# Optimization experiments

Hardware: AMD Instinct MI355X
Metric: run time of the kernel (lower is better)

The kernel has to match this reference:

```python
import jax, jax.numpy as jnp
import numpy as np

N = 8192
IN_DIM = 256
OUT_DIM = 256
NEG_INF = -9e15


def setup_inputs() -> dict:
    key = jax.random.key(0)
    k1, k2, k3, k4, k5 = jax.random.split(key, 5)
    worker_x = jax.random.normal(k1, (N, IN_DIM), dtype=jnp.float32)
    ww_adj = jax.random.randint(k2, (N, N), 0, 2, dtype=jnp.int32)
    # learned params (xavier-ish scales)
    W = jax.random.normal(k3, (IN_DIM, OUT_DIM), dtype=jnp.float32) * (1.0 / np.sqrt(IN_DIM))
    a_src = jax.random.normal(k4, (OUT_DIM, 1), dtype=jnp.float32) * (1.414 / np.sqrt(OUT_DIM))
    a_dst = jax.random.normal(k5, (OUT_DIM, 1), dtype=jnp.float32) * (1.414 / np.sqrt(OUT_DIM))
    return {"worker_x": worker_x, "ww_adj": ww_adj, "W": W, "a_src": a_src, "a_dst": a_dst}


def reference(worker_x, ww_adj, W, a_src, a_dst):
    Wh = worker_x @ W                       # [N, out_dim]
    f_src = Wh @ a_src                      # [N, 1]
    f_dst = Wh @ a_dst                      # [N, 1]
    e = jax.nn.leaky_relu(f_src + f_dst.T, negative_slope=0.2)  # [N, N]
    attention = jnp.where(ww_adj > 0, e, NEG_INF)
    attention = jax.nn.softmax(attention, axis=-1)
    h_prime = attention @ Wh                # [N, out_dim]
    return jax.nn.elu(h_prime)
```

## Files before the change

### kernel.cpp

```cpp
#include <hip/hip_runtime.h>
#include <stdint.h>

typedef __attribute__((ext_vector_type(8))) short short8;
typedef __attribute__((ext_vector_type(4))) float f32x4;
typedef __attribute__((ext_vector_type(4))) _Float16 h16x4;

#define LOG2E 1.4426950408889634f

#define OFF_WTT   0u
#define OFF_WHTB  131072u
#define OFF_BITS  4325376u
#define OFF_FSRC  12713984u
#define OFF_FDST  12746752u
#define OFF_MKEY  12779520u
#define OFF_LP    12779584u
#define OFF_ACCH  13041728u

__device__ __forceinline__ unsigned short f2bf(float f) {
    union { float f; unsigned int i; } v; v.f = f;
    unsigned int u = v.i;
    return (unsigned short)((u + 0x7FFFu + ((u >> 16) & 1u)) >> 16);
}

__global__ void k0_init(const float* __restrict__ W,
                        unsigned short* __restrict__ WTt,
                        unsigned int* __restrict__ Mkey) {
    int idx = blockIdx.x * 256 + threadIdx.x;
    int i = idx >> 8, o = idx & 255;
    WTt[(i >> 5) * 8192 + ((i >> 3) & 3) * 2048 + o * 8 + (i & 7)] = f2bf(W[idx]);
    if (idx == 0) *Mkey = 0u;
}

__global__ __launch_bounds__(256, 8)
void k_pack(const int* __restrict__ adj, unsigned long long* __restrict__ bits64) {
    int wave_id = (blockIdx.x * 256 + threadIdx.x) >> 6;
    int lane = threadIdx.x & 63;
    const int* p = adj + (size_t)wave_id * 16384 + lane;
    unsigned long long* bp = bits64 + (size_t)wave_id * 256;
    for (int it = 0; it < 256; it += 8) {
        int v[8];
#pragma unroll
        for (int u = 0; u < 8; ++u) v[u] = p[(size_t)(it + u) * 64];
#pragma unroll
        for (int u = 0; u < 8; ++u) {
            unsigned long long m = __ballot(v[u] > 0);
            if (lane == 0) bp[it + u] = m;
        }
    }
}

__global__ __launch_bounds__(256, 2)
void k1_stage1(const float* __restrict__ X,
               const unsigned short* __restrict__ WTt,
               const float* __restrict__ a_src,
               const float* __restrict__ a_dst,
               unsigned short* __restrict__ WhTb,
               float* __restrict__ f_src,
               float* __restrict__ f_dst,
               unsigned int* __restrict__ Mkey) {
    __shared__ __align__(16) unsigned short Bt[8192];
    __shared__ float fsum[64];
    const int t = threadIdx.x, w = t >> 6, lane = t & 63, l15 = lane & 15, q = lane >> 4;
    const int rg = w & 1, cg = w >> 1;
    const int i0 = blockIdx.x * 32;
    const int arow = i0 + rg * 16 + l15;

    if (t < 64) fsum[t] = 0.f;

    float as[8], ad[8];
#pragma unroll
    for (int ci = 0; ci < 8; ++ci) {
        int col = cg * 128 + ci * 16 + l15;
        as[ci] = a_src[col]; ad[ci] = a_dst[col];
    }

    f32x4 acc[8];
#pragma unroll
    for (int ci = 0; ci < 8; ++ci) acc[ci] = (f32x4)0.f;

    for (int ks = 0; ks < 8; ++ks) {
        __syncthreads();
        {
            const uint4* src = (const uint4*)(WTt + ks * 8192);
            uint4* dst = (uint4*)Bt;
            dst[t] = src[t]; dst[256 + t] = src[256 + t];
            dst[512 + t] = src[512 + t]; dst[768 + t] = src[768 + t];
        }
        __syncthreads();
        const float* xp = X + (size_t)arow * 256 + ks * 32 + q * 8;
        float4 xa = *(const float4*)xp;
        float4 xb = *(const float4*)(xp + 4);
        short8 a;
        a[0] = (short)f2bf(xa.x); a[1] = (short)f2bf(xa.y);
        a[2] = (short)f2bf(xa.z); a[3] = (short)f2bf(xa.w);
        a[4] = (short)f2bf(xb.x); a[5] = (short)f2bf(xb.y);
        a[6] = (short)f2bf(xb.z); a[7] = (short)f2bf(xb.w);
#pragma unroll
        for (int ci = 0; ci < 8; ++ci) {
            short8 b = *(const short8*)((const char*)Bt + q * 4096 + (cg * 128 + ci * 16 + l15) * 16);
            acc[ci] = __builtin_amdgcn_mfma_f32_16x16x32_bf16(a, b, acc[ci], 0, 0, 0);
        }
    }

#pragma unroll
    for (int ci = 0; ci < 8; ++ci) {
        int col = cg * 128 + ci * 16 + l15;
        ushort4 v;
        v.x = f2bf(acc[ci][0]); v.y = f2bf(acc[ci][1]);
        v.z = f2bf(acc[ci][2]); v.w = f2bf(acc[ci][3]);
        size_t flat = (size_t)(i0 >> 5) * 8192 + (size_t)(rg * 2 + (q >> 1)) * 2048
                      + (size_t)col * 8 + (q & 1) * 4;
        *(ushort4*)(WhTb + flat) = v;
    }

#pragma unroll
    for (int reg = 0; reg < 4; ++reg) {
        float ps = 0.f, pd = 0.f;
#pragma unroll
        for (int ci = 0; ci < 8; ++ci) {
            ps += acc[ci][reg] * as[ci];
            pd += acc[ci][reg] * ad[ci];
        }
#pragma unroll
        for (int m = 1; m < 16; m <<= 1) {
            ps += __shfl_xor(ps, m, 64);
            pd += __shfl_xor(pd, m, 64);
        }
        if (l15 == 0) {
            atomicAdd(&fsum[rg * 16 + q * 4 + reg], ps);
            atomicAdd(&fsum[32 + rg * 16 + q * 4 + reg], pd);
        }
    }
    __syncthreads();
    if (t < 32) {
        int row = i0 + t;
        float ps = fsum[t], pd = fsum[32 + t];
        f_src[row] = ps;
        f_dst[row] = pd;
        union { float f; unsigned int u; } cv; cv.f = pd;
        unsigned int key = (cv.u & 0x80000000u) ? ~cv.u : (cv.u | 0x80000000u);
        atomicMax(Mkey, key);
    }
}

__global__ __launch_bounds__(256, 2)
void k2_flash(const unsigned int* __restrict__ BITS,
              const unsigned short* __restrict__ WhTb,
              const float* __restrict__ f_src,
              const float* __restrict__ f_dst,
              const unsigned int* __restrict__ Mkey,
              float* __restrict__ Lp,
              _Float16* __restrict__ ACCh) {
    __shared__ float fd_s[1024];
    __shared__ unsigned int bits_s[128 * 33];
    const int t = threadIdx.x, w = t >> 6, lane = t & 63, l15 = lane & 15, q = lane >> 4;
    const int i0 = blockIdx.x * 128;
    const int jc = blockIdx.y;
    const int jb0 = jc * 1024;
    const int jw0 = jc * 32;

    { float4* d = (float4*)fd_s; d[t] = ((const float4*)(f_dst + jb0))[t]; }
#pragma unroll
    for (int s = 0; s < 16; ++s) {
        int idx = s * 256 + t;
        int row = idx >> 5, word = idx & 31;
        bits_s[row * 33 + word] = BITS[(size_t)(i0 + row) * 256 + jw0 + word];
    }

    unsigned int key = *Mkey;
    union { unsigned int u; float f; } mv;
    mv.u = (key & 0x80000000u) ? (key & 0x7FFFFFFFu) : ~key;
    const float Mf = mv.f;
    const int rA = i0 + w * 32 + l15;
    const float fsA = f_src[rA], fsB = f_src[rA + 16];
    float vA = fsA + Mf; const float mcA = fmaxf(vA, 0.2f * vA) * LOG2E;
    float vB = fsB + Mf; const float mcB = fmaxf(vB, 0.2f * vB) * LOG2E;
    __syncthreads();

    const unsigned short* Bbase = WhTb + (size_t)jw0 * 8192 + q * 2048 + l15 * 8;
    const unsigned int* brA = &bits_s[(w * 32 + l15) * 33];
    const unsigned int* brB = &bits_s[(w * 32 + 16 + l15) * 33];

    f32x4 accA[16], accB[16];
#pragma unroll
    for (int ci = 0; ci < 16; ++ci) { accA[ci] = (f32x4)0.f; accB[ci] = (f32x4)0.f; }
    float lsA = 0.f, lsB = 0.f;

    for (int js = 0; js < 32; ++js) {
        const float* fdp = fd_s + js * 32 + q * 8;
        float4 f0 = *(const float4*)fdp, f1 = *(const float4*)(fdp + 4);
        float fdv[8] = { f0.x, f0.y, f0.z, f0.w, f1.x, f1.y, f1.z, f1.w };
        unsigned int bA = brA[js] >> (q * 8);
        unsigned int bB = brB[js] >> (q * 8);

        short8 fragA, fragB;
#pragma unroll
        for (int k = 0; k < 8; ++k) {
            float tA = fsA + fdv[k];
            float eA = fmaxf(tA, 0.2f * tA);
            float pA = __builtin_amdgcn_exp2f(__builtin_fmaf(eA, LOG2E, -mcA));
            pA = ((bA >> k) & 1u) ? pA : 0.f;
            lsA += pA; fragA[k] = (short)f2bf(pA);
            float tB = fsB + fdv[k];
            float eB = fmaxf(tB, 0.2f * tB);
            float pB = __builtin_amdgcn_exp2f(__builtin_fmaf(eB, LOG2E, -mcB));
            pB = ((bB >> k) & 1u) ? pB : 0.f;
            lsB += pB; fragB[k] = (short)f2bf(pB);
        }

        const unsigned short* bp = Bbase + (size_t)js * 8192;
        short8 bf[8];
#pragma unroll
        for (int ci = 0; ci < 8; ++ci) bf[ci] = *(const short8*)(bp + ci * 128);
#pragma unroll
        for (int ci = 0; ci < 8; ++ci) {
            accA[ci] = __builtin_amdgcn_mfma_f32_16x16x32_bf16(fragA, bf[ci], accA[ci], 0, 0, 0);
            accB[ci] = __builtin_amdgcn_mfma_f32_16x16x32_bf16(fragB, bf[ci], accB[ci], 0, 0, 0);
        }
#pragma unroll
        for (int ci = 0; ci < 8; ++ci) bf[ci] = *(const short8*)(bp + (ci + 8) * 128);
#pragma unroll
        for (int ci = 0; ci < 8; ++ci) {
            accA[8 + ci] = __builtin_amdgcn_mfma_f32_16x16x32_bf16(fragA, bf[ci], accA[8 + ci], 0, 0, 0);
            accB[8 + ci] = __builtin_amdgcn_mfma_f32_16x16x32_bf16(fragB, bf[ci], accB[8 + ci], 0, 0, 0);
        }
    }

    lsA += __shfl_xor(lsA, 16, 64); lsA += __shfl_xor(lsA, 32, 64);
    lsB += __shfl_xor(lsB, 16, 64); lsB += __shfl_xor(lsB, 32, 64);
    if (lane < 16) {
        Lp[(size_t)jc * 8192 + i0 + w * 32 + lane] = lsA;
        Lp[(size_t)jc * 8192 + i0 + w * 32 + 16 + lane] = lsB;
    }

    _Float16* ap = ACCh + (size_t)jc * 2097152;
#pragma unroll
    for (int ci = 0; ci < 16; ++ci) {
#pragma unroll
        for (int reg = 0; reg < 4; ++reg) {
            int rowA = i0 + w * 32 + q * 4 + reg;
            ap[(size_t)rowA * 256 + ci * 16 + l15] = (_Float16)accA[ci][reg];
            ap[(size_t)(rowA + 16) * 256 + ci * 16 + l15] = (_Float16)accB[ci][reg];
        }
    }
}

__global__ void k4_final(const _Float16* __restrict__ ACCh,
                         const float* __restrict__ Lp,
                         float* __restrict__ out) {
    int gid = blockIdx.x * 256 + threadIdx.x;
    int i = gid >> 6;
    float s0 = 0.f, s1 = 0.f, s2 = 0.f, s3 = 0.f;
#pragma unroll
    for (int jc = 0; jc < 8; ++jc) {
        h16x4 v = *(const h16x4*)(ACCh + (size_t)jc * 2097152 + (size_t)gid * 4);
        s0 += (float)v[0]; s1 += (float)v[1]; s2 += (float)v[2]; s3 += (float)v[3];
    }
    float L = 0.f;
#pragma unroll
    for (int jc = 0; jc < 8; ++jc) L += Lp[jc * 8192 + i];
    float inv = (L > 0.f) ? (1.0f / L) : 0.f;
    float h0 = s0 * inv, h1 = s1 * inv, h2 = s2 * inv, h3 = s3 * inv;
    float4 o;
    o.x = (h0 > 0.f) ? h0 : expm1f(h0);
    o.y = (h1 > 0.f) ? h1 : expm1f(h1);
    o.z = (h2 > 0.f) ? h2 : expm1f(h2);
    o.w = (h3 > 0.f) ? h3 : expm1f(h3);
    *(float4*)(out + (size_t)gid * 4) = o;
}

extern "C" void kernel_launch(void* const* d_in, const int* in_sizes, int n_in,
                              void* d_out, int out_size, void* d_ws, size_t ws_size,
                              hipStream_t stream) {
    (void)in_sizes; (void)n_in; (void)out_size; (void)ws_size;
    const float* X   = (const float*)d_in[0];
    const int*   adj = (const int*)d_in[1];
    const float* W   = (const float*)d_in[2];
    const float* a_s = (const float*)d_in[3];
    const float* a_d = (const float*)d_in[4];

    char* ws = (char*)d_ws;
    unsigned short* WTt  = (unsigned short*)(ws + OFF_WTT);
    unsigned short* WhTb = (unsigned short*)(ws + OFF_WHTB);
    unsigned long long* B64 = (unsigned long long*)(ws + OFF_BITS);
    unsigned int*   BITS = (unsigned int*)(ws + OFF_BITS);
    float*          fsrc = (float*)(ws + OFF_FSRC);
    float*          fdst = (float*)(ws + OFF_FDST);
    unsigned int*   Mkey = (unsigned int*)(ws + OFF_MKEY);
    float*          Lp   = (float*)(ws + OFF_LP);
    _Float16*       ACCh = (_Float16*)(ws + OFF_ACCH);
    float*          out  = (float*)d_out;

    k0_init<<<dim3(256), dim3(256), 0, stream>>>(W, WTt, Mkey);
    k_pack<<<dim3(1024), dim3(256), 0, stream>>>(adj, B64);
    k1_stage1<<<dim3(256), dim3(256), 0, stream>>>(X, WTt, a_s, a_d, WhTb, fsrc, fdst, Mkey);
    k2_flash<<<dim3(64, 8), dim3(256), 0, stream>>>(BITS, WhTb, fsrc, fdst, Mkey, Lp, ACCh);
    k4_final<<<dim3(2048), dim3(256), 0, stream>>>(ACCh, Lp, out);
}
```

Before: 485.5 us.

## Fuse adjacency packing into flash kernel, reading int adjacency directly with prefetch

Drops the separate bit-packing kernel and has the attention kernel read the int32 adjacency matrix directly, prefetching the next step's adjacency and f_dst values into registers. It also drops the shared-memory staging of f_dst and the bitmask, along with the block barrier. This removes one kernel launch and the write and reread of the packed bitmask. In exchange each adjacency element is still read once, but now as 32-bit ints inside the compute-bound kernel, which adds register pressure and may stall the MFMA loop on global loads.

Measured after the change: 469.3 us. -3.3%, faster.

```diff
diff --git a/kernel.cpp b/kernel.cpp
--- a/kernel.cpp
+++ b/kernel.cpp
@@ -9,7 +9,6 @@
 
 #define OFF_WTT   0u
 #define OFF_WHTB  131072u
-#define OFF_BITS  4325376u
 #define OFF_FSRC  12713984u
 #define OFF_FDST  12746752u
 #define OFF_MKEY  12779520u
@@ -29,24 +28,6 @@
     int i = idx >> 8, o = idx & 255;
     WTt[(i >> 5) * 8192 + ((i >> 3) & 3) * 2048 + o * 8 + (i & 7)] = f2bf(W[idx]);
     if (idx == 0) *Mkey = 0u;
-}
-
-__global__ __launch_bounds__(256, 8)
-void k_pack(const int* __restrict__ adj, unsigned long long* __restrict__ bits64) {
-    int wave_id = (blockIdx.x * 256 + threadIdx.x) >> 6;
-    int lane = threadIdx.x & 63;
-    const int* p = adj + (size_t)wave_id * 16384 + lane;
-    unsigned long long* bp = bits64 + (size_t)wave_id * 256;
-    for (int it = 0; it < 256; it += 8) {
-        int v[8];
-#pragma unroll
-        for (int u = 0; u < 8; ++u) v[u] = p[(size_t)(it + u) * 64];
-#pragma unroll
-        for (int u = 0; u < 8; ++u) {
-            unsigned long long m = __ballot(v[u] > 0);
-            if (lane == 0) bp[it + u] = m;
-        }
-    }
 }
 
 __global__ __launch_bounds__(256, 2)
@@ -144,28 +125,18 @@
 }
 
 __global__ __launch_bounds__(256, 2)
-void k2_flash(const unsigned int* __restrict__ BITS,
+void k2_fused(const int* __restrict__ adj,
               const unsigned short* __restrict__ WhTb,
               const float* __restrict__ f_src,
               const float* __restrict__ f_dst,
               const unsigned int* __restrict__ Mkey,
               float* __restrict__ Lp,
               _Float16* __restrict__ ACCh) {
-    __shared__ float fd_s[1024];
-    __shared__ unsigned int bits_s[128 * 33];
     const int t = threadIdx.x, w = t >> 6, lane = t & 63, l15 = lane & 15, q = lane >> 4;
     const int i0 = blockIdx.x * 128;
     const int jc = blockIdx.y;
     const int jb0 = jc * 1024;
     const int jw0 = jc * 32;
-
-    { float4* d = (float4*)fd_s; d[t] = ((const float4*)(f_dst + jb0))[t]; }
-#pragma unroll
-    for (int s = 0; s < 16; ++s) {
-        int idx = s * 256 + t;
-        int row = idx >> 5, word = idx & 31;
-        bits_s[row * 33 + word] = BITS[(size_t)(i0 + row) * 256 + jw0 + word];
-    }
 
     unsigned int key = *Mkey;
     union { unsigned int u; float f; } mv;
@@ -175,23 +146,28 @@
     const float fsA = f_src[rA], fsB = f_src[rA + 16];
     float vA = fsA + Mf; const float mcA = fmaxf(vA, 0.2f * vA) * LOG2E;
     float vB = fsB + Mf; const float mcB = fmaxf(vB, 0.2f * vB) * LOG2E;
-    __syncthreads();
-
+
+    const int* adjA = adj + (size_t)rA * 8192 + jb0 + q * 8;
+    const int* adjB = adj + (size_t)(rA + 16) * 8192 + jb0 + q * 8;
+    const float* fdp = f_dst + jb0 + q * 8;
     const unsigned short* Bbase = WhTb + (size_t)jw0 * 8192 + q * 2048 + l15 * 8;
-    const unsigned int* brA = &bits_s[(w * 32 + l15) * 33];
-    const unsigned int* brB = &bits_s[(w * 32 + 16 + l15) * 33];
 
     f32x4 accA[16], accB[16];
 #pragma unroll
     for (int ci = 0; ci < 16; ++ci) { accA[ci] = (f32x4)0.f; accB[ci] = (f32x4)0.f; }
     float lsA = 0.f, lsB = 0.f;
 
+    int4 pA0 = *(const int4*)(adjA);
+    int4 pA1 = *(const int4*)(adjA + 4);
+    int4 pB0 = *(const int4*)(adjB);
+    int4 pB1 = *(const int4*)(adjB + 4);
+    float4 pf0 = *(const float4*)(fdp);
+    float4 pf1 = *(const float4*)(fdp + 4);
+
     for (int js = 0; js < 32; ++js) {
-        const float* fdp = fd_s + js * 32 + q * 8;
-        float4 f0 = *(const float4*)fdp, f1 = *(const float4*)(fdp + 4);
-        float fdv[8] = { f0.x, f0.y, f0.z, f0.w, f1.x, f1.y, f1.z, f1.w };
-        unsigned int bA = brA[js] >> (q * 8);
-        unsigned int bB = brB[js] >> (q * 8);
+        float fdv[8] = { pf0.x, pf0.y, pf0.z, pf0.w, pf1.x, pf1.y, pf1.z, pf1.w };
+        int aAv[8] = { pA0.x, pA0.y, pA0.z, pA0.w, pA1.x, pA1.y, pA1.z, pA1.w };
+        int aBv[8] = { pB0.x, pB0.y, pB0.z, pB0.w, pB1.x, pB1.y, pB1.z, pB1.w };
 
         short8 fragA, fragB;
 #pragma unroll
@@ -199,14 +175,22 @@
             float tA = fsA + fdv[k];
             float eA = fmaxf(tA, 0.2f * tA);
             float pA = __builtin_amdgcn_exp2f(__builtin_fmaf(eA, LOG2E, -mcA));
-            pA = ((bA >> k) & 1u) ? pA : 0.f;
+            pA = (aAv[k] > 0) ? pA : 0.f;
             lsA += pA; fragA[k] = (short)f2bf(pA);
             float tB = fsB + fdv[k];
             float eB = fmaxf(tB, 0.2f * tB);
             float pB = __builtin_amdgcn_exp2f(__builtin_fmaf(eB, LOG2E, -mcB));
-            pB = ((bB >> k) & 1u) ? pB : 0.f;
+            pB = (aBv[k] > 0) ? pB : 0.f;
             lsB += pB; fragB[k] = (short)f2bf(pB);
         }
+
+        int jn = (js + 1) & 31;
+        pA0 = *(const int4*)(adjA + jn * 32);
+        pA1 = *(const int4*)(adjA + jn * 32 + 4);
+        pB0 = *(const int4*)(adjB + jn * 32);
+        pB1 = *(const int4*)(adjB + jn * 32 + 4);
+        pf0 = *(const float4*)(fdp + jn * 32);
+        pf1 = *(const float4*)(fdp + jn * 32 + 4);
 
         const unsigned short* bp = Bbase + (size_t)js * 8192;
         short8 bf[8];
@@ -282,8 +266,6 @@
     char* ws = (char*)d_ws;
     unsigned short* WTt  = (unsigned short*)(ws + OFF_WTT);
     unsigned short* WhTb = (unsigned short*)(ws + OFF_WHTB);
-    unsigned long long* B64 = (unsigned long long*)(ws + OFF_BITS);
-    unsigned int*   BITS = (unsigned int*)(ws + OFF_BITS);
     float*          fsrc = (float*)(ws + OFF_FSRC);
     float*          fdst = (float*)(ws + OFF_FDST);
     unsigned int*   Mkey = (unsigned int*)(ws + OFF_MKEY);
@@ -292,8 +274,7 @@
     float*          out  = (float*)d_out;
 
     k0_init<<<dim3(256), dim3(256), 0, stream>>>(W, WTt, Mkey);
-    k_pack<<<dim3(1024), dim3(256), 0, stream>>>(adj, B64);
     k1_stage1<<<dim3(256), dim3(256), 0, stream>>>(X, WTt, a_s, a_d, WhTb, fsrc, fdst, Mkey);
-    k2_flash<<<dim3(64, 8), dim3(256), 0, stream>>>(BITS, WhTb, fsrc, fdst, Mkey, Lp, ACCh);
+    k2_fused<<<dim3(64, 8), dim3(256), 0, stream>>>(adj, WhTb, fsrc, fdst, Mkey, Lp, ACCh);
     k4_final<<<dim3(2048), dim3(256), 0, stream>>>(ACCh, Lp, out);
 }
```
